# Optimization experiments

Hardware: AMD Instinct MI355X
Metric: run time of the kernel (lower is better)

The kernel has to match this reference:

```python
import jax, jax.numpy as jnp
import numpy as np

F_DIM, H, B, MAX = 128, 256, 256, 128
N = B * MAX            # 32768 nodes, 256 graphs of 128 nodes each
E = 524288             # avg degree 16
EPS = 1e-5


def _bn(x, g, b):
    # BatchNorm1d in training mode: biased batch stats over the node axis
    m = x.mean(0)
    v = x.var(0)
    return (x - m) * jax.lax.rsqrt(v + EPS) * g + b


def _gcn(x, W, b, src, dst, n):
    # PyG GCNConv: add self-loops, symmetric deg^-1/2 normalization
    h = x @ W
    loops = jnp.arange(n, dtype=src.dtype)
    s = jnp.concatenate([src, loops])
    d = jnp.concatenate([dst, loops])
    deg = jax.ops.segment_sum(jnp.ones_like(s, dtype=x.dtype), d, num_segments=n)
    dinv = jax.lax.rsqrt(jnp.maximum(deg, 1.0))
    norm = dinv[s] * dinv[d]
    out = jax.ops.segment_sum(h[s] * norm[:, None], d, num_segments=n)
    return out + b


def setup_inputs() -> dict:
    key = jax.random.key(0)
    ks = jax.random.split(key, 20)

    def xavier(k, shape, gain=1.414):
        lim = gain * np.sqrt(6.0 / (shape[0] + shape[1]))
        return jax.random.uniform(k, shape, jnp.float32, -lim, lim)

    inp = {}
    inp['x'] = jax.random.normal(ks[0], (N, F_DIM), jnp.float32)
    inp['src_local'] = jax.random.randint(ks[1], (E,), 0, MAX, jnp.int32)
    inp['dst_local'] = jax.random.randint(ks[2], (E,), 0, MAX, jnp.int32)
    dims = [(F_DIM, H), (H, H), (H, H)]
    for i, (di, do) in enumerate(dims):
        inp[f'gcn_w{i}'] = xavier(ks[3 + i], (di, do))
        inp[f'gcn_b{i}'] = jnp.zeros((do,), jnp.float32)
        inp[f'bn_g{i}'] = jnp.ones((do,), jnp.float32)
        inp[f'bn_b{i}'] = jnp.zeros((do,), jnp.float32)
    inp['sc_w0'] = xavier(ks[6], (F_DIM, H), 1.0)
    inp['sc_b0'] = jnp.zeros((H,), jnp.float32)
    inp['edge_w'] = xavier(ks[7], (H, H), 0.01)
    inp['fd_w0'] = xavier(ks[8], (H, H)); inp['fd_b0'] = jnp.zeros((H,), jnp.float32)
    inp['fd_g0'] = jnp.ones((H,), jnp.float32); inp['fd_be0'] = jnp.zeros((H,), jnp.float32)
    inp['fd_w1'] = xavier(ks[9], (H, H)); inp['fd_b1'] = jnp.zeros((H,), jnp.float32)
    inp['fd_g1'] = jnp.ones((H,), jnp.float32); inp['fd_be1'] = jnp.zeros((H,), jnp.float32)
    inp['fd_w2'] = xavier(ks[10], (H, F_DIM)); inp['fd_b2'] = jnp.zeros((F_DIM,), jnp.float32)
    inp['ph_w0'] = xavier(ks[11], (H, H)); inp['ph_b0'] = jnp.zeros((H,), jnp.float32)
    inp['ph_w1'] = xavier(ks[12], (H, H)); inp['ph_b1'] = jnp.zeros((H,), jnp.float32)
    return inp


def reference(x, src_local, dst_local,
              gcn_w0, gcn_b0, bn_g0, bn_b0, sc_w0, sc_b0,
              gcn_w1, gcn_b1, bn_g1, bn_b1,
              gcn_w2, gcn_b2, bn_g2, bn_b2,
              edge_w,
              fd_w0, fd_b0, fd_g0, fd_be0,
              fd_w1, fd_b1, fd_g1, fd_be1,
              fd_w2, fd_b2,
              ph_w0, ph_b0, ph_w1, ph_b1):
    n = x.shape[0]
    # global edge index: edge e belongs to graph e // (E//B); offset by g*MAX
    off = (jnp.arange(E, dtype=jnp.int32) // (E // B)) * MAX
    src = src_local + off
    dst = dst_local + off

    def block(h, W, b, g, bb, shortcut):
        res = shortcut(h)
        out = jax.nn.relu(_bn(_gcn(h, W, b, src, dst, n), g, bb))
        return jax.nn.relu(out + res)  # dropout is identity at inference

    z = block(x, gcn_w0, gcn_b0, bn_g0, bn_b0, lambda h: h @ sc_w0 + sc_b0)
    z = block(z, gcn_w1, gcn_b1, bn_g1, bn_b1, lambda h: h)
    z = block(z, gcn_w2, gcn_b2, bn_g2, bn_b2, lambda h: h)
    # F.normalize(p=2, dim=1)
    z = z / jnp.maximum(jnp.linalg.norm(z, axis=1, keepdims=True), 1e-12)

    # BilinearEdgeDecoder per graph, vectorized: sigmoid(Z W Z^T) with zero diag
    zb = z.reshape(B, MAX, H)
    adj = jax.nn.sigmoid(jnp.einsum('bnd,de,bme->bnm', zb, edge_w, zb))
    adj = adj * (1.0 - jnp.eye(MAX, dtype=adj.dtype))

    # Feature_Decoder: [Linear,ReLU,BN] x2 then Linear
    h = _bn(jax.nn.relu(z @ fd_w0 + fd_b0), fd_g0, fd_be0)
    h = _bn(jax.nn.relu(h @ fd_w1 + fd_b1), fd_g1, fd_be1)
    x_recon = h @ fd_w2 + fd_b2

    z_g = zb.max(axis=1)  # global_max_pool per graph
    z_g_mlp = jax.nn.relu(z_g @ ph_w0 + ph_b0) @ ph_w1 + ph_b1
    return (z, adj, x_recon, z_g, z_g_mlp)
```

## Files before the change

kernel.cpp:

```cpp
#include <hip/hip_runtime.h>
#include <hip/hip_bf16.h>

using bf = __hip_bfloat16;
typedef __attribute__((ext_vector_type(8))) short s8;
typedef __attribute__((ext_vector_type(4))) float f4;

constexpr int NN  = 32768;
constexpr int HD  = 256;

__device__ __forceinline__ float u2f(unsigned short h) {
    union { unsigned u; float f; } x; x.u = ((unsigned)h) << 16;
    return x.f;
}
__device__ __forceinline__ unsigned short f2u(float f) {
    union { float f; unsigned u; } x; x.f = f;
    unsigned r = x.u + 0x7FFF + ((x.u >> 16) & 1);
    return (unsigned short)(r >> 16);
}
__device__ __forceinline__ bf f2bf(float f) {
    unsigned short h = f2u(f);
    return *reinterpret_cast<bf*>(&h);
}
__device__ __forceinline__ float bf2f(bf b) {
    return u2f(*reinterpret_cast<unsigned short*>(&b));
}

__device__ __forceinline__ int swz(int row, int slot) {
    return row * 64 + ((slot ^ (row & 7)) << 3);
}
__device__ __forceinline__ int swz128(int row, int slot) {
    return row * 128 + ((slot ^ (row & 7)) << 3);
}

struct WTd { const float* src; int K, N, off; };
struct WTpack { WTd w[10]; };

__global__ __launch_bounds__(256) void k_prep(const int* __restrict__ srcL,
                                              const int* __restrict__ dstL,
                                              const float* __restrict__ xf,
                                              WTpack p, bf* __restrict__ A,
                                              bf* __restrict__ xb,
                                              bf* __restrict__ wT) {
    __shared__ __align__(16) float shm[8320];
    int b = blockIdx.x, t = threadIdx.x;
    if (b < 256) {
        float* sT = shm;
        float* sdin = shm + 8192;
        int g = b;
        const int* sg = srcL + (g << 11);
        const int* dg = dstL + (g << 11);
        if (t < 128) sdin[t] = 0.f;
        __syncthreads();
        for (int e = t; e < 2048; e += 256) atomicAdd(&sdin[dg[e]], 1.0f);
        __syncthreads();
        if (t < 128) sdin[t] = rsqrtf(sdin[t] + 1.0f);
        __syncthreads();
        bf* out = A + ((long)g << 14);
        for (int half = 0; half < 2; ++half) {
            for (int i = t; i < 8192; i += 256) sT[i] = 0.f;
            __syncthreads();
            for (int e = t; e < 2048; e += 256) {
                int s = sg[e], d = dg[e];
                if ((s >> 6) == half)
                    atomicAdd(&sT[(d << 6) + (s & 63)], sdin[s] * sdin[d]);
            }
            __syncthreads();
            if (t < 128 && (t >> 6) == half)
                sT[(t << 6) + (t & 63)] += sdin[t] * sdin[t];
            __syncthreads();
            for (int i4 = t; i4 < 2048; i4 += 256) {
                int d = i4 >> 4, c4 = (i4 & 15) * 4;
                float4 v = *(float4*)&sT[(d << 6) + c4];
                ushort4 u = make_ushort4(f2u(v.x), f2u(v.y), f2u(v.z), f2u(v.w));
                *(ushort4*)&out[(d << 7) + (half << 6) + c4] = u;
            }
            __syncthreads();
        }
    } else if (b < 416) {
        int idx = b - 256;
        WTd d = p.w[idx >> 4];
        int rem = idx & 15;
        int n0 = (rem & 3) * 64, k0 = (rem >> 2) * 64;
        if (n0 >= d.N || k0 >= d.K) return;
        float (*s)[65] = (float(*)[65])shm;
        int cc = t & 63, rq = t >> 6;
#pragma unroll
        for (int i = 0; i < 16; ++i) {
            int r = i * 4 + rq;
            s[r][cc] = d.src[(long)(k0 + r) * d.N + n0 + cc];
        }
        __syncthreads();
#pragma unroll
        for (int i = 0; i < 16; ++i) {
            int r = i * 4 + rq;
            wT[d.off + (long)(n0 + r) * d.K + k0 + cc] = f2bf(s[cc][r]);
        }
    } else {
        long base = (long)(b - 416) * 16384;
#pragma unroll
        for (int it = 0; it < 16; ++it) {
            long i4 = base + (it * 256 + t) * 4;
            float4 v = *(const float4*)&xf[i4];
            *(ushort4*)&xb[i4] = make_ushort4(f2u(v.x), f2u(v.y), f2u(v.z), f2u(v.w));
        }
    }
}

template <int EPI, int OUT, bool PART, bool BNA, bool AF32>
__global__ __launch_bounds__(256) void mg(
    const void* __restrict__ Av, const bf* __restrict__ BT,
    const float* __restrict__ bias, const float* __restrict__ bnstats,
    float* __restrict__ Cf, bf* __restrict__ Cb, float* __restrict__ part,
    int M, int N, int K, int ldc) {
    __shared__ __align__(16) bf sAl[128 * 64];
    __shared__ __align__(16) bf sBl[128 * 64];
    const int m0 = blockIdx.y * 128, n0 = blockIdx.x * 128;
    const bf* Bb = BT + (long)n0 * K;
    const int t = threadIdx.x;
    const int lane = t & 63;
    const int w = t >> 6;
    const int wm = (w >> 1) * 64, wn = (w & 1) * 64;
    const int fr16 = lane & 15, kq = lane >> 4;
    f4 acc[4][4] = {};
    for (int k0 = 0; k0 < K; k0 += 64) {
#pragma unroll
        for (int i = 0; i < 4; ++i) {
            int sdx = i * 256 + t;
            int row = sdx >> 3, sl = sdx & 7;
            s8 av;
            if constexpr (AF32) {
                const float* src = (const float*)Av + (long)(m0 + row) * K + k0 + sl * 8;
                float4 f0 = *(const float4*)src;
                float4 f1 = *(const float4*)(src + 4);
                unsigned short u[8] = {f2u(f0.x), f2u(f0.y), f2u(f0.z), f2u(f0.w),
                                       f2u(f1.x), f2u(f1.y), f2u(f1.z), f2u(f1.w)};
                av = *(s8*)u;
            } else {
                av = *(const s8*)&((const bf*)Av)[(long)(m0 + row) * K + k0 + sl * 8];
                if constexpr (BNA) {
                    int c = k0 + sl * 8;
                    float4 sc0 = *(const float4*)&bnstats[c];
                    float4 sc1 = *(const float4*)&bnstats[c + 4];
                    float4 sh0 = *(const float4*)&bnstats[256 + c];
                    float4 sh1 = *(const float4*)&bnstats[256 + c + 4];
                    float scv[8] = {sc0.x, sc0.y, sc0.z, sc0.w, sc1.x, sc1.y, sc1.z, sc1.w};
                    float shv[8] = {sh0.x, sh0.y, sh0.z, sh0.w, sh1.x, sh1.y, sh1.z, sh1.w};
                    unsigned short* u = (unsigned short*)&av;
#pragma unroll
                    for (int j = 0; j < 8; ++j)
                        u[j] = f2u(fmaf(u2f(u[j]), scv[j], shv[j]));
                }
            }
            *(s8*)&sAl[swz(row, sl)] = av;
            *(s8*)&sBl[swz(row, sl)] = *(const s8*)&Bb[(long)row * K + k0 + sl * 8];
        }
        __syncthreads();
#pragma unroll
        for (int ks = 0; ks < 2; ++ks) {
            s8 af[4], bg[4];
#pragma unroll
            for (int f = 0; f < 4; ++f) {
                af[f] = *(const s8*)&sAl[swz(wm + f * 16 + fr16, kq + 4 * ks)];
                bg[f] = *(const s8*)&sBl[swz(wn + f * 16 + fr16, kq + 4 * ks)];
            }
#pragma unroll
            for (int fr = 0; fr < 4; ++fr)
#pragma unroll
                for (int fc = 0; fc < 4; ++fc)
                    acc[fr][fc] = __builtin_amdgcn_mfma_f32_16x16x32_bf16(
                        af[fr], bg[fc], acc[fr][fc], 0, 0, 0);
        }
        __syncthreads();
    }
    float ps[4], ps2[4];
    if (PART) {
#pragma unroll
        for (int fc = 0; fc < 4; ++fc) { ps[fc] = 0.f; ps2[fc] = 0.f; }
    }
#pragma unroll
    for (int fr = 0; fr < 4; ++fr) {
        int rl = wm + fr * 16 + (lane >> 4) * 4;
#pragma unroll
        for (int fc = 0; fc < 4; ++fc) {
            int cl = wn + fc * 16 + (lane & 15);
            int col = n0 + cl;
            float bv = bias[col];
#pragma unroll
            for (int i = 0; i < 4; ++i) {
                float v = acc[fr][fc][i] + bv;
                if (EPI == 2) v = fmaxf(v, 0.f);
                if (PART) { ps[fc] += v; ps2[fc] += v * v; }
                if (OUT == 0) Cf[(long)(m0 + rl + i) * ldc + col] = v;
                if (OUT == 1) Cb[(long)(m0 + rl + i) * ldc + col] = f2bf(v);
            }
        }
    }
    if (PART) {
        __syncthreads();
        float* scr = (float*)sAl;
#pragma unroll
        for (int fc = 0; fc < 4; ++fc) {
            ps[fc] += __shfl_xor(ps[fc], 16);  ps[fc] += __shfl_xor(ps[fc], 32);
            ps2[fc] += __shfl_xor(ps2[fc], 16); ps2[fc] += __shfl_xor(ps2[fc], 32);
        }
        if (lane < 16) {
#pragma unroll
            for (int fc = 0; fc < 4; ++fc) {
                scr[(w * 2 + 0) * 64 + fc * 16 + lane] = ps[fc];
                scr[(w * 2 + 1) * 64 + fc * 16 + lane] = ps2[fc];
            }
        }
        __syncthreads();
        int id = blockIdx.x * gridDim.y + blockIdx.y;
        int stat = t >> 7, c = t & 127;
        int ci = c & 63, half = c >> 6;
        float v = scr[(half * 2 + stat) * 64 + ci] + scr[((half + 2) * 2 + stat) * 64 + ci];
        part[(long)id * 256 + stat * 128 + c] = v;
    }
}

template <int MODE>
__global__ __launch_bounds__(512) void k_fused(
    const bf* __restrict__ Xin,
    const bf* __restrict__ Res, const float* __restrict__ stats,
    const bf* __restrict__ Wt, const bf* __restrict__ Wt2,
    const float* __restrict__ scb, const bf* __restrict__ Adj,
    bf* __restrict__ Zout, bf* __restrict__ AG, bf* __restrict__ ResOut,
    float* __restrict__ part, float* __restrict__ adjout) {
    __shared__ __align__(16) bf sOut[128 * 128];
    __shared__ __align__(16) bf sStg[128 * 128];
    const int g = blockIdx.x;
    const int hb = blockIdx.y;
    const int t = threadIdx.x;
    const int lane = t & 63, w = t >> 6;
    const int wm = w >> 2, wn = w & 3;
    const int l15 = lane & 15, kq = lane >> 4;
    constexpr int KS1 = (MODE == 2) ? 128 : 256;
    const int h0 = (MODE == 1) ? 0 : hb;
    const int h1 = (MODE == 1) ? 2 : hb + 1;
    const bf* Xg = Xin + (long)g * ((MODE == 2) ? 16384 : 32768);
    const bf* Rg = (MODE == 0) ? Res + (long)g * 32768 : nullptr;
    f4 acc2[4][2] = {};
    for (int h = h0; h < h1; ++h) {
        f4 acc1[4][2] = {};
        for (int k0 = 0; k0 < KS1; k0 += 64) {
            __syncthreads();
#pragma unroll
            for (int i = 0; i < 2; ++i) {
                int sdx = i * 512 + t;
                int row = sdx >> 3, sl = sdx & 7;
                int c = k0 + sl * 8;
                s8 av;
                if constexpr (MODE == 0) {
                    av = *(const s8*)&Xg[row * 256 + c];
                    s8 rv = *(const s8*)&Rg[row * 256 + c];
                    float4 sc0 = *(const float4*)&stats[c];
                    float4 sc1 = *(const float4*)&stats[c + 4];
                    float4 sh0 = *(const float4*)&stats[256 + c];
                    float4 sh1 = *(const float4*)&stats[256 + c + 4];
                    float scv[8] = {sc0.x, sc0.y, sc0.z, sc0.w, sc1.x, sc1.y, sc1.z, sc1.w};
                    float shv[8] = {sh0.x, sh0.y, sh0.z, sh0.w, sh1.x, sh1.y, sh1.z, sh1.w};
                    unsigned short* u = (unsigned short*)&av;
                    const unsigned short* ru = (const unsigned short*)&rv;
#pragma unroll
                    for (int j = 0; j < 8; ++j) {
                        float v = fmaf(u2f(u[j]), scv[j], shv[j]);
                        v = fmaxf(v, 0.f) + u2f(ru[j]);
                        u[j] = f2u(fmaxf(v, 0.f));
                    }
                    if (h == 0)
                        *(s8*)&Zout[(long)g * 32768 + row * 256 + c] = av;
                } else if constexpr (MODE == 2) {
                    av = *(const s8*)&Xg[row * 128 + c];
                } else {
                    av = *(const s8*)&Wt[(h * 128 + row) * 256 + c];
                }
                *(s8*)&sStg[swz(row, sl)] = av;
                s8 bv;
                if constexpr (MODE == 0)
                    bv = *(const s8*)&Wt[(h * 128 + row) * 256 + c];
                else if constexpr (MODE == 2) {
                    const bf* Wsrc = (h < 2) ? Wt : Wt2;
                    bv = *(const s8*)&Wsrc[((h & 1) * 128 + row) * 128 + c];
                } else
                    bv = *(const s8*)&Xg[row * 256 + c];
                *(s8*)&sStg[8192 + swz(row, sl)] = bv;
            }
            __syncthreads();
#pragma unroll
            for (int ks = 0; ks < 2; ++ks) {
                s8 af[4], bg[2];
#pragma unroll
                for (int f = 0; f < 4; ++f)
                    af[f] = *(const s8*)&sStg[swz(wm * 64 + f * 16 + l15, kq + 4 * ks)];
#pragma unroll
                for (int f = 0; f < 2; ++f)
                    bg[f] = *(const s8*)&sStg[8192 + swz(wn * 32 + f * 16 + l15, kq + 4 * ks)];
#pragma unroll
                for (int fr = 0; fr < 4; ++fr)
#pragma unroll
                    for (int fc = 0; fc < 2; ++fc)
                        acc1[fr][fc] = __builtin_amdgcn_mfma_f32_16x16x32_bf16(
                            af[fr], bg[fc], acc1[fr][fc], 0, 0, 0);
            }
        }
        if (MODE == 2 && h >= 2) {
#pragma unroll
            for (int fr = 0; fr < 4; ++fr) {
                int rl = wm * 64 + fr * 16 + kq * 4;
#pragma unroll
                for (int fc = 0; fc < 2; ++fc) {
                    int cl = wn * 32 + fc * 16 + l15;
                    float bv = scb[(h - 2) * 128 + cl];
#pragma unroll
                    for (int i = 0; i < 4; ++i)
                        ResOut[(long)(g * 128 + rl + i) * 256 + (h - 2) * 128 + cl] =
                            f2bf(acc1[fr][fc][i] + bv);
                }
            }
            continue;
        }
#pragma unroll
        for (int fr = 0; fr < 4; ++fr) {
            int rl = wm * 64 + fr * 16 + kq * 4;
#pragma unroll
            for (int fc = 0; fc < 2; ++fc) {
                int cl = wn * 32 + fc * 16 + l15;
                ushort4 q = make_ushort4(f2u(acc1[fr][fc][0]), f2u(acc1[fr][fc][1]),
                                         f2u(acc1[fr][fc][2]), f2u(acc1[fr][fc][3]));
                int off = cl * 128 + (((rl >> 3) ^ (cl & 7)) << 3) + (rl & 7);
                *(ushort4*)&sOut[off] = q;
            }
        }
        __syncthreads();
#pragma unroll
        for (int i = 0; i < 4; ++i) {
            int sdx = i * 512 + t;
            int row = sdx >> 4, sl = sdx & 15;
            const bf* src = (MODE == 1)
                ? Xg + row * 256 + h * 128 + sl * 8
                : Adj + ((long)g << 14) + row * 128 + sl * 8;
            *(s8*)&sStg[swz128(row, sl)] = *(const s8*)src;
        }
        __syncthreads();
        if (MODE != 1) {
#pragma unroll
            for (int fr = 0; fr < 4; ++fr)
#pragma unroll
                for (int fc = 0; fc < 2; ++fc) acc2[fr][fc] = f4{0.f, 0.f, 0.f, 0.f};
        }
#pragma unroll
        for (int ks = 0; ks < 4; ++ks) {
            s8 af[4], bg[2];
#pragma unroll
            for (int f = 0; f < 4; ++f)
                af[f] = *(const s8*)&sStg[swz128(wm * 64 + f * 16 + l15, ks * 4 + kq)];
#pragma unroll
            for (int f = 0; f < 2; ++f)
                bg[f] = *(const s8*)&sOut[swz128(wn * 32 + f * 16 + l15, ks * 4 + kq)];
#pragma unroll
            for (int fr = 0; fr < 4; ++fr)
#pragma unroll
                for (int fc = 0; fc < 2; ++fc)
                    acc2[fr][fc] = __builtin_amdgcn_mfma_f32_16x16x32_bf16(
                        af[fr], bg[fc], acc2[fr][fc], 0, 0, 0);
        }
        if (MODE != 1) {
            float ps[2] = {0.f, 0.f}, ps2[2] = {0.f, 0.f};
#pragma unroll
            for (int fr = 0; fr < 4; ++fr) {
                int rl = wm * 64 + fr * 16 + kq * 4;
#pragma unroll
                for (int fc = 0; fc < 2; ++fc) {
                    int cl = wn * 32 + fc * 16 + l15;
#pragma unroll
                    for (int i = 0; i < 4; ++i) {
                        float v = acc2[fr][fc][i];
                        ps[fc] += v; ps2[fc] += v * v;
                        AG[(long)(g * 128 + rl + i) * 256 + h * 128 + cl] = f2bf(v);
                    }
                }
            }
            __syncthreads();
            float* scr = (float*)sStg;
#pragma unroll
            for (int fc = 0; fc < 2; ++fc) {
                ps[fc] += __shfl_xor(ps[fc], 16);  ps[fc] += __shfl_xor(ps[fc], 32);
                ps2[fc] += __shfl_xor(ps2[fc], 16); ps2[fc] += __shfl_xor(ps2[fc], 32);
            }
            if (lane < 16) {
#pragma unroll
                for (int fc = 0; fc < 2; ++fc) {
                    int c = wn * 32 + fc * 16 + lane;
                    scr[(c * 2 + wm) * 2 + 0] = ps[fc];
                    scr[(c * 2 + wm) * 2 + 1] = ps2[fc];
                }
            }
            __syncthreads();
            if (t < 256) {
                int col = t & 127, s = t >> 7;
                part[(long)(h * 256 + g) * 256 + s * 128 + col] =
                    scr[(col * 2 + 0) * 2 + s] + scr[(col * 2 + 1) * 2 + s];
            }
        }
        if (MODE == 1 && h == 1) {
#pragma unroll
            for (int fr = 0; fr < 4; ++fr) {
                int rl = wm * 64 + fr * 16 + kq * 4;
#pragma unroll
                for (int fc = 0; fc < 2; ++fc) {
                    int cl = wn * 32 + fc * 16 + l15;
                    float vv[4];
#pragma unroll
                    for (int i = 0; i < 4; ++i) {
                        float v = 1.f / (1.f + __expf(-acc2[fr][fc][i]));
                        if (cl == rl + i) v = 0.f;
                        vv[i] = v;
                    }
                    float4 o; o.x = vv[0]; o.y = vv[1]; o.z = vv[2]; o.w = vv[3];
                    *(float4*)&adjout[((long)g << 14) + cl * 128 + rl] = o;
                }
            }
        }
    }
}

__global__ void k_bnfin(const float* __restrict__ part, const float* __restrict__ gam,
                        const float* __restrict__ bet, float* __restrict__ stats) {
    int ch = blockIdx.x;
    int half = ch >> 7, cc = ch & 127;
    int t = threadIdx.x;
    __shared__ float2 sm[256];
    const float* p = part + (long)(half * 256 + t) * 256;
    sm[t] = make_float2(p[cc], p[128 + cc]);
    __syncthreads();
    for (int s = 128; s > 0; s >>= 1) {
        if (t < s) { sm[t].x += sm[t + s].x; sm[t].y += sm[t + s].y; }
        __syncthreads();
    }
    if (t == 0) {
        float m = sm[0].x / (float)NN;
        float var = sm[0].y / (float)NN - m * m;
        float sc = rsqrtf(var + 1e-5f) * gam[ch];
        stats[ch]       = sc;
        stats[256 + ch] = bet[ch] - m * sc;
    }
}

__global__ __launch_bounds__(512) void k_finz(
    const bf* __restrict__ X, const float* __restrict__ stats,
    const bf* __restrict__ res, float* __restrict__ outz, bf* __restrict__ Znb,
    unsigned* __restrict__ zgu) {
    int g = blockIdx.x, half = blockIdx.y;
    int t = threadIdx.x;
    int lane = t & 63, w = t >> 6;
    int c4 = lane * 4;
    float4 sc = *(const float4*)&stats[c4];
    float4 sh = *(const float4*)&stats[256 + c4];
    float scv[4] = {sc.x, sc.y, sc.z, sc.w};
    float shv[4] = {sh.x, sh.y, sh.z, sh.w};
    float cmax[4] = {0.f, 0.f, 0.f, 0.f};
#pragma unroll
    for (int it = 0; it < 8; ++it) {
        int r = half * 64 + w * 8 + it;
        long i = (long)(g * 128 + r) * 256 + c4;
        ushort4 xv = *(const ushort4*)(X + i);
        ushort4 rv = *(const ushort4*)(res + i);
        unsigned short xs[4] = {xv.x, xv.y, xv.z, xv.w};
        unsigned short rs[4] = {rv.x, rv.y, rv.z, rv.w};
        float v[4];
        float s = 0.f;
#pragma unroll
        for (int j = 0; j < 4; ++j) {
            float vv = fmaf(u2f(xs[j]), scv[j], shv[j]);
            vv = fmaxf(vv, 0.f) + u2f(rs[j]);
            vv = fmaxf(vv, 0.f);
            v[j] = vv;
            s += vv * vv;
        }
#pragma unroll
        for (int o = 1; o < 64; o <<= 1) s += __shfl_xor(s, o);
        float den = fmaxf(sqrtf(s), 1e-12f);
        float4 fo;
        unsigned short us[4];
#pragma unroll
        for (int j = 0; j < 4; ++j) {
            float o = v[j] / den;
            ((float*)&fo)[j] = o;
            us[j] = f2u(o);
            cmax[j] = fmaxf(cmax[j], o);
        }
        *(float4*)(outz + i) = fo;
        *(ushort4*)(Znb + i) = make_ushort4(us[0], us[1], us[2], us[3]);
    }
    __shared__ float pm[8][256];
#pragma unroll
    for (int j = 0; j < 4; ++j) pm[w][c4 + j] = cmax[j];
    __syncthreads();
    if (t < 256) {
        float m = pm[0][t];
#pragma unroll
        for (int ww = 1; ww < 8; ++ww) m = fmaxf(m, pm[ww][t]);
        atomicMax(&zgu[g * 256 + t], __float_as_uint(m));
    }
}

template <int EPI, int OUT, bool PART, bool BNA, bool AF32>
static void MG(hipStream_t st, const void* A, const bf* BT, const float* bias,
               const float* bnstats, float* Cf, bf* Cb, float* part,
               int M, int N, int K, int ldc) {
    dim3 g(N / 128, M / 128, 1);
    mg<EPI, OUT, PART, BNA, AF32><<<g, 256, 0, st>>>(A, BT, bias, bnstats, Cf, Cb, part,
                                                     M, N, K, ldc);
}

extern "C" void kernel_launch(void* const* d_in, const int* in_sizes, int n_in,
                              void* d_out, int out_size, void* d_ws, size_t ws_size,
                              hipStream_t stream) {
    const float* x      = (const float*)d_in[0];
    const int*   srcL   = (const int*)d_in[1];
    const int*   dstL   = (const int*)d_in[2];
    const float* gcn_w0 = (const float*)d_in[3];
    const float* bn_g0  = (const float*)d_in[5];
    const float* bn_b0  = (const float*)d_in[6];
    const float* gcn_w1 = (const float*)d_in[7];
    const float* bn_g1  = (const float*)d_in[9];
    const float* bn_b1  = (const float*)d_in[10];
    const float* gcn_w2 = (const float*)d_in[11];
    const float* bn_g2  = (const float*)d_in[13];
    const float* bn_b2  = (const float*)d_in[14];
    const float* sc_w0  = (const float*)d_in[15];
    const float* sc_b0  = (const float*)d_in[16];
    const float* edge_w = (const float*)d_in[17];
    const float* fd_w0  = (const float*)d_in[18];
    const float* fd_b0  = (const float*)d_in[19];
    const float* fd_g0  = (const float*)d_in[20];
    const float* fd_be0 = (const float*)d_in[21];
    const float* fd_w1  = (const float*)d_in[22];
    const float* fd_b1  = (const float*)d_in[23];
    const float* fd_g1  = (const float*)d_in[24];
    const float* fd_be1 = (const float*)d_in[25];
    const float* fd_w2  = (const float*)d_in[26];
    const float* fd_b2  = (const float*)d_in[27];
    const float* ph_w0  = (const float*)d_in[28];
    const float* ph_b0  = (const float*)d_in[29];
    const float* ph_w1  = (const float*)d_in[30];
    const float* ph_b1  = (const float*)d_in[31];

    float* out     = (float*)d_out;
    float* out_z   = out;
    float* out_adj = out + 8388608;
    float* out_xr  = out + 12582912;
    float* out_zg  = out + 16777216;
    float* out_zgm = out + 16842752;

    float* w     = (float*)d_ws;
    float* part  = w;
    float* stats = w + 131072;
    bf*    wT    = (bf*)(w + 131584);
    bf*    Aadjb = (bf*)(w + 410112);
    bf*    U4    = (bf*)(w + 2507264);
    bf*    U1    = (bf*)(w + 6701568);
    bf*    U2    = (bf*)(w + 10895872);
    bf*    U3    = (bf*)(w + 15090176);
    bf*    P1b   = (bf*)(w + 19284480);
    bf*    xb    = (bf*)(w + 19317248);

    WTpack pk;
    pk.w[0] = {gcn_w0, 128, 256, 0};
    pk.w[1] = {sc_w0,  128, 256, 32768};
    pk.w[2] = {gcn_w1, 256, 256, 65536};
    pk.w[3] = {gcn_w2, 256, 256, 131072};
    pk.w[4] = {edge_w, 256, 256, 196608};
    pk.w[5] = {fd_w0,  256, 256, 262144};
    pk.w[6] = {fd_w1,  256, 256, 327680};
    pk.w[7] = {fd_w2,  256, 128, 393216};
    pk.w[8] = {ph_w0,  256, 256, 425984};
    pk.w[9] = {ph_w1,  256, 256, 491520};

    hipMemsetAsync(out_zg, 0, 65536 * 4, stream);

    k_prep<<<672, 256, 0, stream>>>(srcL, dstL, x, pk, Aadjb, xb, wT);

    k_fused<2><<<dim3(256, 4), 512, 0, stream>>>(xb, nullptr, nullptr,
                                                 wT + 0, wT + 32768, sc_b0, Aadjb,
                                                 nullptr, U2, U1, part, nullptr);
    k_bnfin<<<256, 256, 0, stream>>>(part, bn_g0, bn_b0, stats);

    k_fused<0><<<dim3(256, 2), 512, 0, stream>>>(U2, U1, stats,
                                                 wT + 65536, nullptr, nullptr, Aadjb,
                                                 U3, U4, nullptr, part, nullptr);
    k_bnfin<<<256, 256, 0, stream>>>(part, bn_g1, bn_b1, stats);

    k_fused<0><<<dim3(256, 2), 512, 0, stream>>>(U4, U3, stats,
                                                 wT + 131072, nullptr, nullptr, Aadjb,
                                                 U1, U2, nullptr, part, nullptr);
    k_bnfin<<<256, 256, 0, stream>>>(part, bn_g2, bn_b2, stats);

    k_finz<<<dim3(256, 2), 512, 0, stream>>>(U2, stats, U1, out_z, U3,
                                             (unsigned*)out_zg);

    k_fused<1><<<dim3(256, 1), 512, 0, stream>>>(U3, nullptr, nullptr,
                                                 wT + 196608, nullptr, nullptr, nullptr,
                                                 nullptr, nullptr, nullptr, nullptr,
                                                 out_adj);

    MG<2, 1, true, false, false>(stream, U3, wT + 262144, fd_b0, nullptr,
                                 nullptr, U4, part, NN, HD, HD, 256);
    k_bnfin<<<256, 256, 0, stream>>>(part, fd_g0, fd_be0, stats);
    MG<2, 1, true, true, false>(stream, U4, wT + 327680, fd_b1, stats,
                                nullptr, U2, part, NN, HD, HD, 256);
    k_bnfin<<<256, 256, 0, stream>>>(part, fd_g1, fd_be1, stats);
    MG<1, 0, false, true, false>(stream, U2, wT + 393216, fd_b2, stats,
                                 out_xr, nullptr, nullptr, NN, 128, HD, 128);

    MG<2, 1, false, false, true>(stream, out_zg, wT + 425984, ph_b0, nullptr,
                                 nullptr, P1b, nullptr, 256, 256, 256, 256);
    MG<1, 0, false, false, false>(stream, P1b, wT + 491520, ph_b1, nullptr,
                                  out_zgm, nullptr, nullptr, 256, 256, 256, 256);
}
```

Before: 182.6 us.

## Fuse edge decoder with first feature-decoder layer and use direct global-to-LDS loads

Splits the templated fused GCN kernel into per-mode code, replacing several register-staged tile loads with global_load_lds direct-to-LDS transfers using a pre-swizzled source address. The bilinear edge decoder and the first feature-decoder linear layer, which used a separate generic GEMM launch, now share one kernel: 256 blocks run the decoder and 512 blocks run the per-graph linear layer with ReLU and BN partial statistics. This removes a launch and lets the two independent workloads run concurrently. In exchange the feature-decoder layer now uses 128x128 per-graph tiles instead of the generic GEMM, and its part layout must match what k_bnfin expects.

```diff
diff --git a/kernel.cpp b/kernel.cpp
--- a/kernel.cpp
+++ b/kernel.cpp
@@ -30,6 +30,12 @@
 }
 __device__ __forceinline__ int swz128(int row, int slot) {
     return row * 128 + ((slot ^ (row & 7)) << 3);
+}
+
+typedef const __attribute__((address_space(1))) unsigned int guint;
+typedef __attribute__((address_space(3))) unsigned int luint;
+__device__ __forceinline__ void gload16(const void* g, void* l) {
+    __builtin_amdgcn_global_load_lds((guint*)g, (luint*)l, 16, 0, 0);
 }
 
 struct WTd { const float* src; int K, N, off; };
@@ -102,6 +108,322 @@
             long i4 = base + (it * 256 + t) * 4;
             float4 v = *(const float4*)&xf[i4];
             *(ushort4*)&xb[i4] = make_ushort4(f2u(v.x), f2u(v.y), f2u(v.z), f2u(v.w));
+        }
+    }
+}
+
+__device__ __forceinline__ void mfma_s1(const bf* sA, const bf* sB, f4 (&acc)[4][2],
+                                        int wm, int wn, int l15, int kq) {
+#pragma unroll
+    for (int ks = 0; ks < 2; ++ks) {
+        s8 af[4], bg[2];
+#pragma unroll
+        for (int f = 0; f < 4; ++f)
+            af[f] = *(const s8*)&sA[swz(wm * 64 + f * 16 + l15, kq + 4 * ks)];
+#pragma unroll
+        for (int f = 0; f < 2; ++f)
+            bg[f] = *(const s8*)&sB[swz(wn * 32 + f * 16 + l15, kq + 4 * ks)];
+#pragma unroll
+        for (int fr = 0; fr < 4; ++fr)
+#pragma unroll
+            for (int fc = 0; fc < 2; ++fc)
+                acc[fr][fc] = __builtin_amdgcn_mfma_f32_16x16x32_bf16(
+                    af[fr], bg[fc], acc[fr][fc], 0, 0, 0);
+    }
+}
+
+__device__ __forceinline__ void mfma_s2(const bf* sA, const bf* sB, f4 (&acc)[4][2],
+                                        int wm, int wn, int l15, int kq) {
+#pragma unroll
+    for (int ks = 0; ks < 4; ++ks) {
+        s8 af[4], bg[2];
+#pragma unroll
+        for (int f = 0; f < 4; ++f)
+            af[f] = *(const s8*)&sA[swz128(wm * 64 + f * 16 + l15, ks * 4 + kq)];
+#pragma unroll
+        for (int f = 0; f < 2; ++f)
+            bg[f] = *(const s8*)&sB[swz128(wn * 32 + f * 16 + l15, ks * 4 + kq)];
+#pragma unroll
+        for (int fr = 0; fr < 4; ++fr)
+#pragma unroll
+            for (int fc = 0; fc < 2; ++fc)
+                acc[fr][fc] = __builtin_amdgcn_mfma_f32_16x16x32_bf16(
+                    af[fr], bg[fc], acc[fr][fc], 0, 0, 0);
+    }
+}
+
+__device__ __forceinline__ void tstore(bf* sOut, f4 (&acc)[4][2],
+                                       int wm, int wn, int l15, int kq) {
+#pragma unroll
+    for (int fr = 0; fr < 4; ++fr) {
+        int rl = wm * 64 + fr * 16 + kq * 4;
+#pragma unroll
+        for (int fc = 0; fc < 2; ++fc) {
+            int cl = wn * 32 + fc * 16 + l15;
+            ushort4 q = make_ushort4(f2u(acc[fr][fc][0]), f2u(acc[fr][fc][1]),
+                                     f2u(acc[fr][fc][2]), f2u(acc[fr][fc][3]));
+            int off = cl * 128 + (((rl >> 3) ^ (cl & 7)) << 3) + (rl & 7);
+            *(ushort4*)&sOut[off] = q;
+        }
+    }
+}
+
+template <int MODE>
+__global__ __launch_bounds__(512) void k_fused(
+    const bf* __restrict__ Xin,
+    const bf* __restrict__ Res, const float* __restrict__ stats,
+    const bf* __restrict__ Wt, const bf* __restrict__ Wt2,
+    const float* __restrict__ scb, const bf* __restrict__ Adj,
+    bf* __restrict__ Zout, bf* __restrict__ AG, bf* __restrict__ ResOut,
+    float* __restrict__ part) {
+    __shared__ __align__(16) bf sOut[16384];
+    __shared__ __align__(16) bf sStg[16384];
+    const int g = blockIdx.x;
+    const int h = blockIdx.y;
+    const int t = threadIdx.x;
+    const int lane = t & 63, w = t >> 6;
+    const int wm = w >> 2, wn = w & 3;
+    const int l15 = lane & 15, kq = lane >> 4;
+    constexpr int KS1 = (MODE == 2) ? 128 : 256;
+    const bf* Xg = Xin + (long)g * ((MODE == 2) ? 16384 : 32768);
+    const bf* Rg = (MODE == 0) ? Res + (long)g * 32768 : nullptr;
+
+    f4 acc1[4][2] = {};
+    for (int k0 = 0; k0 < KS1; k0 += 64) {
+        __syncthreads();
+#pragma unroll
+        for (int i = 0; i < 2; ++i) {
+            if constexpr (MODE == 0) {
+                int sdx = i * 512 + t;
+                int row = sdx >> 3, sl = sdx & 7;
+                int c = k0 + sl * 8;
+                s8 av = *(const s8*)&Xg[row * 256 + c];
+                s8 rv = *(const s8*)&Rg[row * 256 + c];
+                float4 sc0 = *(const float4*)&stats[c];
+                float4 sc1 = *(const float4*)&stats[c + 4];
+                float4 sh0 = *(const float4*)&stats[256 + c];
+                float4 sh1 = *(const float4*)&stats[256 + c + 4];
+                float scv[8] = {sc0.x, sc0.y, sc0.z, sc0.w, sc1.x, sc1.y, sc1.z, sc1.w};
+                float shv[8] = {sh0.x, sh0.y, sh0.z, sh0.w, sh1.x, sh1.y, sh1.z, sh1.w};
+                unsigned short* u = (unsigned short*)&av;
+                const unsigned short* ru = (const unsigned short*)&rv;
+#pragma unroll
+                for (int j = 0; j < 8; ++j) {
+                    float v = fmaf(u2f(u[j]), scv[j], shv[j]);
+                    v = fmaxf(v, 0.f) + u2f(ru[j]);
+                    u[j] = f2u(fmaxf(v, 0.f));
+                }
+                if (h == 0)
+                    *(s8*)&Zout[(long)g * 32768 + row * 256 + c] = av;
+                *(s8*)&sStg[swz(row, sl)] = av;
+            } else {
+                int r0 = i * 64 + 8 * w;
+                int rw = r0 + (lane >> 3);
+                int ps = ((lane & 7) ^ (rw & 7)) << 3;
+                gload16(&Xg[rw * 128 + k0 + ps], &sStg[r0 * 64]);
+            }
+            {
+                int r0 = i * 64 + 8 * w;
+                int rw = r0 + (lane >> 3);
+                int ps = ((lane & 7) ^ (rw & 7)) << 3;
+                const bf* bsrc;
+                if constexpr (MODE == 0)
+                    bsrc = &Wt[(h * 128 + rw) * 256 + k0 + ps];
+                else {
+                    const bf* Wsrc = (h < 2) ? Wt : Wt2;
+                    bsrc = &Wsrc[((h & 1) * 128 + rw) * 128 + k0 + ps];
+                }
+                gload16(bsrc, &sStg[8192 + r0 * 64]);
+            }
+        }
+        __syncthreads();
+        mfma_s1(sStg, sStg + 8192, acc1, wm, wn, l15, kq);
+    }
+    if (MODE == 2 && h >= 2) {
+#pragma unroll
+        for (int fr = 0; fr < 4; ++fr) {
+            int rl = wm * 64 + fr * 16 + kq * 4;
+#pragma unroll
+            for (int fc = 0; fc < 2; ++fc) {
+                int cl = wn * 32 + fc * 16 + l15;
+                float bv = scb[(h - 2) * 128 + cl];
+#pragma unroll
+                for (int i = 0; i < 4; ++i)
+                    ResOut[(long)(g * 128 + rl + i) * 256 + (h - 2) * 128 + cl] =
+                        f2bf(acc1[fr][fc][i] + bv);
+            }
+        }
+        return;
+    }
+    tstore(sOut, acc1, wm, wn, l15, kq);
+    __syncthreads();
+#pragma unroll
+    for (int i = 0; i < 4; ++i) {
+        int r0 = i * 32 + 4 * w;
+        int rw = r0 + (lane >> 4);
+        int ps = ((lane & 15) ^ (rw & 7)) << 3;
+        gload16(&Adj[((long)g << 14) + rw * 128 + ps], &sStg[r0 * 128]);
+    }
+    __syncthreads();
+    f4 acc2[4][2] = {};
+    mfma_s2(sStg, sOut, acc2, wm, wn, l15, kq);
+    float ps[2] = {0.f, 0.f}, ps2[2] = {0.f, 0.f};
+#pragma unroll
+    for (int fr = 0; fr < 4; ++fr) {
+        int rl = wm * 64 + fr * 16 + kq * 4;
+#pragma unroll
+        for (int fc = 0; fc < 2; ++fc) {
+            int cl = wn * 32 + fc * 16 + l15;
+#pragma unroll
+            for (int i = 0; i < 4; ++i) {
+                float v = acc2[fr][fc][i];
+                ps[fc] += v; ps2[fc] += v * v;
+                AG[(long)(g * 128 + rl + i) * 256 + (h & 1) * 128 + cl] = f2bf(v);
+            }
+        }
+    }
+    __syncthreads();
+    float* scr = (float*)sStg;
+#pragma unroll
+    for (int fc = 0; fc < 2; ++fc) {
+        ps[fc] += __shfl_xor(ps[fc], 16);  ps[fc] += __shfl_xor(ps[fc], 32);
+        ps2[fc] += __shfl_xor(ps2[fc], 16); ps2[fc] += __shfl_xor(ps2[fc], 32);
+    }
+    if (lane < 16) {
+#pragma unroll
+        for (int fc = 0; fc < 2; ++fc) {
+            int c = wn * 32 + fc * 16 + lane;
+            scr[(c * 2 + wm) * 2 + 0] = ps[fc];
+            scr[(c * 2 + wm) * 2 + 1] = ps2[fc];
+        }
+    }
+    __syncthreads();
+    if (t < 256) {
+        int col = t & 127, s = t >> 7;
+        part[(long)((h & 1) * 256 + g) * 256 + s * 128 + col] =
+            scr[(col * 2 + 0) * 2 + s] + scr[(col * 2 + 1) * 2 + s];
+    }
+}
+
+__device__ __forceinline__ void fd_layer(const bf* Zg, const bf* W, const float* bias,
+                                         bf* C, float* part, bf* sStg,
+                                         int g, int h, int t, int lane,
+                                         int wm, int wn, int l15, int kq) {
+    f4 acc[4][2] = {};
+    for (int k0 = 0; k0 < 256; k0 += 64) {
+        __syncthreads();
+#pragma unroll
+        for (int i = 0; i < 2; ++i) {
+            int sdx = i * 512 + t;
+            int row = sdx >> 3, sl = sdx & 7;
+            int c = k0 + sl * 8;
+            *(s8*)&sStg[swz(row, sl)] = *(const s8*)&Zg[row * 256 + c];
+            *(s8*)&sStg[8192 + swz(row, sl)] = *(const s8*)&W[(h * 128 + row) * 256 + c];
+        }
+        __syncthreads();
+        mfma_s1(sStg, sStg + 8192, acc, wm, wn, l15, kq);
+    }
+    float ps[2] = {0.f, 0.f}, ps2[2] = {0.f, 0.f};
+#pragma unroll
+    for (int fr = 0; fr < 4; ++fr) {
+        int rl = wm * 64 + fr * 16 + kq * 4;
+#pragma unroll
+        for (int fc = 0; fc < 2; ++fc) {
+            int cl = wn * 32 + fc * 16 + l15;
+            float bv = bias[h * 128 + cl];
+#pragma unroll
+            for (int i = 0; i < 4; ++i) {
+                float v = fmaxf(acc[fr][fc][i] + bv, 0.f);
+                ps[fc] += v; ps2[fc] += v * v;
+                C[(long)(g * 128 + rl + i) * 256 + h * 128 + cl] = f2bf(v);
+            }
+        }
+    }
+    __syncthreads();
+    float* scr = (float*)sStg;
+#pragma unroll
+    for (int fc = 0; fc < 2; ++fc) {
+        ps[fc] += __shfl_xor(ps[fc], 16);  ps[fc] += __shfl_xor(ps[fc], 32);
+        ps2[fc] += __shfl_xor(ps2[fc], 16); ps2[fc] += __shfl_xor(ps2[fc], 32);
+    }
+    if (lane < 16) {
+#pragma unroll
+        for (int fc = 0; fc < 2; ++fc) {
+            int c = wn * 32 + fc * 16 + lane;
+            scr[(c * 2 + wm) * 2 + 0] = ps[fc];
+            scr[(c * 2 + wm) * 2 + 1] = ps2[fc];
+        }
+    }
+    __syncthreads();
+    if (t < 256) {
+        int col = t & 127, s = t >> 7;
+        part[(long)(h * 256 + g) * 256 + s * 128 + col] =
+            scr[(col * 2 + 0) * 2 + s] + scr[(col * 2 + 1) * 2 + s];
+    }
+}
+
+__global__ __launch_bounds__(512) void k_edfd(
+    const bf* __restrict__ Zn, const bf* __restrict__ ewT,
+    const bf* __restrict__ fdw, const float* __restrict__ fdb,
+    float* __restrict__ adjout, bf* __restrict__ C, float* __restrict__ part) {
+    __shared__ __align__(16) bf sOut[16384];
+    __shared__ __align__(16) bf sStg[16384];
+    const int t = threadIdx.x;
+    const int lane = t & 63, w = t >> 6;
+    const int wm = w >> 2, wn = w & 3;
+    const int l15 = lane & 15, kq = lane >> 4;
+    if (blockIdx.x >= 256) {
+        int bb = blockIdx.x - 256;
+        int g = bb & 255, h = bb >> 8;
+        fd_layer(Zn + (long)g * 32768, fdw, fdb, C, part, sStg,
+                 g, h, t, lane, wm, wn, l15, kq);
+        return;
+    }
+    const int g = blockIdx.x;
+    const bf* Xg = Zn + (long)g * 32768;
+    f4 acc2[4][2] = {};
+    for (int h = 0; h < 2; ++h) {
+        f4 acc1[4][2] = {};
+        for (int k0 = 0; k0 < 256; k0 += 64) {
+            __syncthreads();
+#pragma unroll
+            for (int i = 0; i < 2; ++i) {
+                int sdx = i * 512 + t;
+                int row = sdx >> 3, sl = sdx & 7;
+                int c = k0 + sl * 8;
+                *(s8*)&sStg[swz(row, sl)] = *(const s8*)&ewT[(h * 128 + row) * 256 + c];
+                *(s8*)&sStg[8192 + swz(row, sl)] = *(const s8*)&Xg[row * 256 + c];
+            }
+            __syncthreads();
+            mfma_s1(sStg, sStg + 8192, acc1, wm, wn, l15, kq);
+        }
+        tstore(sOut, acc1, wm, wn, l15, kq);
+        __syncthreads();
+#pragma unroll
+        for (int i = 0; i < 4; ++i) {
+            int sdx = i * 512 + t;
+            int row = sdx >> 4, sl = sdx & 15;
+            *(s8*)&sStg[swz128(row, sl)] = *(const s8*)&Xg[row * 256 + h * 128 + sl * 8];
+        }
+        __syncthreads();
+        mfma_s2(sStg, sOut, acc2, wm, wn, l15, kq);
+        __syncthreads();
+    }
+#pragma unroll
+    for (int fr = 0; fr < 4; ++fr) {
+        int rl = wm * 64 + fr * 16 + kq * 4;
+#pragma unroll
+        for (int fc = 0; fc < 2; ++fc) {
+            int cl = wn * 32 + fc * 16 + l15;
+            float vv[4];
+#pragma unroll
+            for (int i = 0; i < 4; ++i) {
+                float v = 1.f / (1.f + __expf(-acc2[fr][fc][i]));
+                if (cl == rl + i) v = 0.f;
+                vv[i] = v;
+            }
+            float4 o; o.x = vv[0]; o.y = vv[1]; o.z = vv[2]; o.w = vv[3];
+            *(float4*)&adjout[((long)g << 14) + cl * 128 + rl] = o;
         }
     }
 }
@@ -216,212 +538,6 @@
         int ci = c & 63, half = c >> 6;
         float v = scr[(half * 2 + stat) * 64 + ci] + scr[((half + 2) * 2 + stat) * 64 + ci];
         part[(long)id * 256 + stat * 128 + c] = v;
-    }
-}
-
-template <int MODE>
-__global__ __launch_bounds__(512) void k_fused(
-    const bf* __restrict__ Xin,
-    const bf* __restrict__ Res, const float* __restrict__ stats,
-    const bf* __restrict__ Wt, const bf* __restrict__ Wt2,
-    const float* __restrict__ scb, const bf* __restrict__ Adj,
-    bf* __restrict__ Zout, bf* __restrict__ AG, bf* __restrict__ ResOut,
-    float* __restrict__ part, float* __restrict__ adjout) {
-    __shared__ __align__(16) bf sOut[128 * 128];
-    __shared__ __align__(16) bf sStg[128 * 128];
-    const int g = blockIdx.x;
-    const int hb = blockIdx.y;
-    const int t = threadIdx.x;
-    const int lane = t & 63, w = t >> 6;
-    const int wm = w >> 2, wn = w & 3;
-    const int l15 = lane & 15, kq = lane >> 4;
-    constexpr int KS1 = (MODE == 2) ? 128 : 256;
-    const int h0 = (MODE == 1) ? 0 : hb;
-    const int h1 = (MODE == 1) ? 2 : hb + 1;
-    const bf* Xg = Xin + (long)g * ((MODE == 2) ? 16384 : 32768);
-    const bf* Rg = (MODE == 0) ? Res + (long)g * 32768 : nullptr;
-    f4 acc2[4][2] = {};
-    for (int h = h0; h < h1; ++h) {
-        f4 acc1[4][2] = {};
-        for (int k0 = 0; k0 < KS1; k0 += 64) {
-            __syncthreads();
-#pragma unroll
-            for (int i = 0; i < 2; ++i) {
-                int sdx = i * 512 + t;
-                int row = sdx >> 3, sl = sdx & 7;
-                int c = k0 + sl * 8;
-                s8 av;
-                if constexpr (MODE == 0) {
-                    av = *(const s8*)&Xg[row * 256 + c];
-                    s8 rv = *(const s8*)&Rg[row * 256 + c];
-                    float4 sc0 = *(const float4*)&stats[c];
-                    float4 sc1 = *(const float4*)&stats[c + 4];
-                    float4 sh0 = *(const float4*)&stats[256 + c];
-                    float4 sh1 = *(const float4*)&stats[256 + c + 4];
-                    float scv[8] = {sc0.x, sc0.y, sc0.z, sc0.w, sc1.x, sc1.y, sc1.z, sc1.w};
-                    float shv[8] = {sh0.x, sh0.y, sh0.z, sh0.w, sh1.x, sh1.y, sh1.z, sh1.w};
-                    unsigned short* u = (unsigned short*)&av;
-                    const unsigned short* ru = (const unsigned short*)&rv;
-#pragma unroll
-                    for (int j = 0; j < 8; ++j) {
-                        float v = fmaf(u2f(u[j]), scv[j], shv[j]);
-                        v = fmaxf(v, 0.f) + u2f(ru[j]);
-                        u[j] = f2u(fmaxf(v, 0.f));
-                    }
-                    if (h == 0)
-                        *(s8*)&Zout[(long)g * 32768 + row * 256 + c] = av;
-                } else if constexpr (MODE == 2) {
-                    av = *(const s8*)&Xg[row * 128 + c];
-                } else {
-                    av = *(const s8*)&Wt[(h * 128 + row) * 256 + c];
-                }
-                *(s8*)&sStg[swz(row, sl)] = av;
-                s8 bv;
-                if constexpr (MODE == 0)
-                    bv = *(const s8*)&Wt[(h * 128 + row) * 256 + c];
-                else if constexpr (MODE == 2) {
-                    const bf* Wsrc = (h < 2) ? Wt : Wt2;
-                    bv = *(const s8*)&Wsrc[((h & 1) * 128 + row) * 128 + c];
-                } else
-                    bv = *(const s8*)&Xg[row * 256 + c];
-                *(s8*)&sStg[8192 + swz(row, sl)] = bv;
-            }
-            __syncthreads();
-#pragma unroll
-            for (int ks = 0; ks < 2; ++ks) {
-                s8 af[4], bg[2];
-#pragma unroll
-                for (int f = 0; f < 4; ++f)
-                    af[f] = *(const s8*)&sStg[swz(wm * 64 + f * 16 + l15, kq + 4 * ks)];
-#pragma unroll
-                for (int f = 0; f < 2; ++f)
-                    bg[f] = *(const s8*)&sStg[8192 + swz(wn * 32 + f * 16 + l15, kq + 4 * ks)];
-#pragma unroll
-                for (int fr = 0; fr < 4; ++fr)
-#pragma unroll
-                    for (int fc = 0; fc < 2; ++fc)
-                        acc1[fr][fc] = __builtin_amdgcn_mfma_f32_16x16x32_bf16(
-                            af[fr], bg[fc], acc1[fr][fc], 0, 0, 0);
-            }
-        }
-        if (MODE == 2 && h >= 2) {
-#pragma unroll
-            for (int fr = 0; fr < 4; ++fr) {
-                int rl = wm * 64 + fr * 16 + kq * 4;
-#pragma unroll
-                for (int fc = 0; fc < 2; ++fc) {
-                    int cl = wn * 32 + fc * 16 + l15;
-                    float bv = scb[(h - 2) * 128 + cl];
-#pragma unroll
-                    for (int i = 0; i < 4; ++i)
-                        ResOut[(long)(g * 128 + rl + i) * 256 + (h - 2) * 128 + cl] =
-                            f2bf(acc1[fr][fc][i] + bv);
-                }
-            }
-            continue;
-        }
-#pragma unroll
-        for (int fr = 0; fr < 4; ++fr) {
-            int rl = wm * 64 + fr * 16 + kq * 4;
-#pragma unroll
-            for (int fc = 0; fc < 2; ++fc) {
-                int cl = wn * 32 + fc * 16 + l15;
-                ushort4 q = make_ushort4(f2u(acc1[fr][fc][0]), f2u(acc1[fr][fc][1]),
-                                         f2u(acc1[fr][fc][2]), f2u(acc1[fr][fc][3]));
-                int off = cl * 128 + (((rl >> 3) ^ (cl & 7)) << 3) + (rl & 7);
-                *(ushort4*)&sOut[off] = q;
-            }
-        }
-        __syncthreads();
-#pragma unroll
-        for (int i = 0; i < 4; ++i) {
-            int sdx = i * 512 + t;
-            int row = sdx >> 4, sl = sdx & 15;
-            const bf* src = (MODE == 1)
-                ? Xg + row * 256 + h * 128 + sl * 8
-                : Adj + ((long)g << 14) + row * 128 + sl * 8;
-            *(s8*)&sStg[swz128(row, sl)] = *(const s8*)src;
-        }
-        __syncthreads();
-        if (MODE != 1) {
-#pragma unroll
-            for (int fr = 0; fr < 4; ++fr)
-#pragma unroll
-                for (int fc = 0; fc < 2; ++fc) acc2[fr][fc] = f4{0.f, 0.f, 0.f, 0.f};
-        }
-#pragma unroll
-        for (int ks = 0; ks < 4; ++ks) {
-            s8 af[4], bg[2];
-#pragma unroll
-            for (int f = 0; f < 4; ++f)
-                af[f] = *(const s8*)&sStg[swz128(wm * 64 + f * 16 + l15, ks * 4 + kq)];
-#pragma unroll
-            for (int f = 0; f < 2; ++f)
-                bg[f] = *(const s8*)&sOut[swz128(wn * 32 + f * 16 + l15, ks * 4 + kq)];
-#pragma unroll
-            for (int fr = 0; fr < 4; ++fr)
-#pragma unroll
-                for (int fc = 0; fc < 2; ++fc)
-                    acc2[fr][fc] = __builtin_amdgcn_mfma_f32_16x16x32_bf16(
-                        af[fr], bg[fc], acc2[fr][fc], 0, 0, 0);
-        }
-        if (MODE != 1) {
-            float ps[2] = {0.f, 0.f}, ps2[2] = {0.f, 0.f};
-#pragma unroll
-            for (int fr = 0; fr < 4; ++fr) {
-                int rl = wm * 64 + fr * 16 + kq * 4;
-#pragma unroll
-                for (int fc = 0; fc < 2; ++fc) {
-                    int cl = wn * 32 + fc * 16 + l15;
-#pragma unroll
-                    for (int i = 0; i < 4; ++i) {
-                        float v = acc2[fr][fc][i];
-                        ps[fc] += v; ps2[fc] += v * v;
-                        AG[(long)(g * 128 + rl + i) * 256 + h * 128 + cl] = f2bf(v);
-                    }
-                }
-            }
-            __syncthreads();
-            float* scr = (float*)sStg;
-#pragma unroll
-            for (int fc = 0; fc < 2; ++fc) {
-                ps[fc] += __shfl_xor(ps[fc], 16);  ps[fc] += __shfl_xor(ps[fc], 32);
-                ps2[fc] += __shfl_xor(ps2[fc], 16); ps2[fc] += __shfl_xor(ps2[fc], 32);
-            }
-            if (lane < 16) {
-#pragma unroll
-                for (int fc = 0; fc < 2; ++fc) {
-                    int c = wn * 32 + fc * 16 + lane;
-                    scr[(c * 2 + wm) * 2 + 0] = ps[fc];
-                    scr[(c * 2 + wm) * 2 + 1] = ps2[fc];
-                }
-            }
-            __syncthreads();
-            if (t < 256) {
-                int col = t & 127, s = t >> 7;
-                part[(long)(h * 256 + g) * 256 + s * 128 + col] =
-                    scr[(col * 2 + 0) * 2 + s] + scr[(col * 2 + 1) * 2 + s];
-            }
-        }
-        if (MODE == 1 && h == 1) {
-#pragma unroll
-            for (int fr = 0; fr < 4; ++fr) {
-                int rl = wm * 64 + fr * 16 + kq * 4;
-#pragma unroll
-                for (int fc = 0; fc < 2; ++fc) {
-                    int cl = wn * 32 + fc * 16 + l15;
-                    float vv[4];
-#pragma unroll
-                    for (int i = 0; i < 4; ++i) {
-                        float v = 1.f / (1.f + __expf(-acc2[fr][fc][i]));
-                        if (cl == rl + i) v = 0.f;
-                        vv[i] = v;
-                    }
-                    float4 o; o.x = vv[0]; o.y = vv[1]; o.z = vv[2]; o.w = vv[3];
-                    *(float4*)&adjout[((long)g << 14) + cl * 128 + rl] = o;
-                }
-            }
-        }
     }
 }
 
@@ -584,30 +700,26 @@
 
     k_fused<2><<<dim3(256, 4), 512, 0, stream>>>(xb, nullptr, nullptr,
                                                  wT + 0, wT + 32768, sc_b0, Aadjb,
-                                                 nullptr, U2, U1, part, nullptr);
+                                                 nullptr, U2, U1, part);
     k_bnfin<<<256, 256, 0, stream>>>(part, bn_g0, bn_b0, stats);
 
     k_fused<0><<<dim3(256, 2), 512, 0, stream>>>(U2, U1, stats,
                                                  wT + 65536, nullptr, nullptr, Aadjb,
-                                                 U3, U4, nullptr, part, nullptr);
+                                                 U3, U4, nullptr, part);
     k_bnfin<<<256, 256, 0, stream>>>(part, bn_g1, bn_b1, stats);
 
     k_fused<0><<<dim3(256, 2), 512, 0, stream>>>(U4, U3, stats,
                                                  wT + 131072, nullptr, nullptr, Aadjb,
-                                                 U1, U2, nullptr, part, nullptr);
+                                                 U1, U2, nullptr, part);
     k_bnfin<<<256, 256, 0, stream>>>(part, bn_g2, bn_b2, stats);
 
     k_finz<<<dim3(256, 2), 512, 0, stream>>>(U2, stats, U1, out_z, U3,
                                              (unsigned*)out_zg);
 
-    k_fused<1><<<dim3(256, 1), 512, 0, stream>>>(U3, nullptr, nullptr,
-                                                 wT + 196608, nullptr, nullptr, nullptr,
-                                                 nullptr, nullptr, nullptr, nullptr,
-                                                 out_adj);
-
-    MG<2, 1, true, false, false>(stream, U3, wT + 262144, fd_b0, nullptr,
-                                 nullptr, U4, part, NN, HD, HD, 256);
+    k_edfd<<<768, 512, 0, stream>>>(U3, wT + 196608, wT + 262144, fd_b0,
+                                    out_adj, U4, part);
     k_bnfin<<<256, 256, 0, stream>>>(part, fd_g0, fd_be0, stats);
+
     MG<2, 1, true, true, false>(stream, U4, wT + 327680, fd_b1, stats,
                                 nullptr, U2, part, NN, HD, HD, 256);
     k_bnfin<<<256, 256, 0, stream>>>(part, fd_g1, fd_be1, stats);
```

New measurement: 182.8 us. No clear change (+0.1%).
